# Kernel optimization log

Hardware: AMD Instinct MI355X
Metric: run time of the kernel (lower is better)

The kernel has to match this reference:

```python
import jax, jax.numpy as jnp
import numpy as np

EPS = 1e-5
NUM_CLUSTERS = 64


def _bn(x, g, b, m, v):
    # eval-mode BatchNorm over channel (last) axis
    return (x - m) * (g * jax.lax.rsqrt(v + EPS)) + b


def _segment_max(feat, choice, num_clusters):
    # feat: [B, N, C], choice: [B, N] -> [B, K, C] (amax per cluster, -inf if empty)
    def one(f, c):
        init = jnp.full((num_clusters, f.shape[-1]), -jnp.inf, dtype=f.dtype)
        return init.at[c].max(f)
    return jax.vmap(one)(feat, choice)


def setup_inputs() -> dict:
    key = jax.random.key(0)
    ks = jax.random.split(key, 8)
    B, N, K, OUT = 32, 8192, NUM_CLUSTERS, 384
    s = lambda fan: 1.0 / np.sqrt(fan)
    return {
        "xyz": jax.random.normal(ks[0], (B, N, 3), jnp.float32),
        "choice": jax.random.randint(ks[1], (B, N), 0, K, jnp.int32),
        "w1": jax.random.normal(ks[2], (128, 3), jnp.float32) * s(3),
        "b1": jnp.zeros((128,), jnp.float32),
        "bn1_g": jnp.ones((128,), jnp.float32),
        "bn1_b": jnp.zeros((128,), jnp.float32),
        "bn1_m": jnp.zeros((128,), jnp.float32),
        "bn1_v": jnp.ones((128,), jnp.float32),
        "w2": jax.random.normal(ks[3], (256, 128), jnp.float32) * s(128),
        "b2": jnp.zeros((256,), jnp.float32),
        "w3": jax.random.normal(ks[4], (512, 512), jnp.float32) * s(512),
        "b3": jnp.zeros((512,), jnp.float32),
        "bn2_g": jnp.ones((512,), jnp.float32),
        "bn2_b": jnp.zeros((512,), jnp.float32),
        "bn2_m": jnp.zeros((512,), jnp.float32),
        "bn2_v": jnp.ones((512,), jnp.float32),
        "w4": jax.random.normal(ks[5], (OUT, 512), jnp.float32) * s(512),
        "b4": jnp.zeros((OUT,), jnp.float32),
    }


def reference(xyz, choice, w1, b1, bn1_g, bn1_b, bn1_m, bn1_v, w2, b2,
              w3, b3, bn2_g, bn2_b, bn2_m, bn2_v, w4, b4):
    # first_conv: 1x1 conv == per-point linear. xyz: [B,N,3]
    h = jnp.einsum("bnc,oc->bno", xyz, w1) + b1            # [B,N,128]
    h = jax.nn.relu(_bn(h, bn1_g, bn1_b, bn1_m, bn1_v))
    feat = jnp.einsum("bnc,oc->bno", h, w2) + b2            # [B,N,256]
    # cluster amax pooling + gather-broadcast back to points
    fg = _segment_max(feat, choice, NUM_CLUSTERS)           # [B,K,256]
    fg_pts = jnp.take_along_axis(fg, choice[..., None], axis=1)  # [B,N,256]
    f = jnp.concatenate([fg_pts, feat], axis=-1)            # [B,N,512]
    # second_conv
    h2 = jnp.einsum("bnc,oc->bno", f, w3) + b3              # [B,N,512]
    h2 = jax.nn.relu(_bn(h2, bn2_g, bn2_b, bn2_m, bn2_v))
    out = jnp.einsum("bnc,oc->bno", h2, w4) + b4            # [B,N,out_dim]
    return _segment_max(out, choice, NUM_CLUSTERS)          # [B,K,out_dim]
```

## Files before the change

### kernel.cpp

```cpp
#include <hip/hip_runtime.h>
#include <hip/hip_bf16.h>

typedef unsigned short u16;
typedef __attribute__((ext_vector_type(8))) short short8;
typedef __attribute__((ext_vector_type(4))) float f32x4;

#define EPSV 1e-5f
#define ENC_NINF 0x007FFFFFu

__device__ __forceinline__ float bf2f(u16 u) {
    union { unsigned int i; float f; } v; v.i = ((unsigned int)u) << 16; return v.f;
}
__device__ __forceinline__ u16 f2bf(float f) {
    union { float f; unsigned int i; } v; v.f = f;
    unsigned int x = v.i;
    return (u16)((x + 0x7FFFu + ((x >> 16) & 1u)) >> 16);
}
__device__ __forceinline__ unsigned int encbf(u16 u) {
    unsigned int f = ((unsigned int)u) << 16;
    return (f & 0x80000000u) ? ~f : (f | 0x80000000u);
}
__device__ __forceinline__ float dec(unsigned int u) {
    union { float f; unsigned int uu; } v;
    v.uu = (u & 0x80000000u) ? (u & 0x7FFFFFFFu) : ~u;
    return v.f;
}

__device__ __forceinline__ void async16(const u16* g, u16* l) {
    __builtin_amdgcn_global_load_lds((const __attribute__((address_space(1))) void*)g,
                                     (__attribute__((address_space(3))) void*)l,
                                     16, 0, 0);
}

__global__ __launch_bounds__(256) void k_fillf(float* __restrict__ o, int n, float val)
{
    int i = blockIdx.x * 256 + threadIdx.x;
    if (i < n) o[i] = val;
}

__global__ __launch_bounds__(256) void k_initu(unsigned int* __restrict__ o, int n)
{
    int i = blockIdx.x * 256 + threadIdx.x;
    if (i < n) o[i] = ENC_NINF;
}

struct Ptrs { const void* p[17]; int off[18]; int chN; };

__global__ __launch_bounds__(256) void k_repack(Ptrs P, const void* __restrict__ chSrc,
                                                int* __restrict__ chi, u16* __restrict__ rp)
{
    const unsigned int* probe = (const unsigned int*)P.p[9];
    int cnt = 0;
#pragma unroll
    for (int i = 0; i < 64; ++i) {
        unsigned int lo = probe[i] & 0xFFFFu;
        if (((lo >> 7) & 0xFFu) >= 0x80u) ++cnt;
    }
    const bool is_f32 = (cnt > 8);

    const unsigned int* cp = (const unsigned int*)chSrc;
    int z = 0; unsigned int mx = 0;
    for (int i = 0; i < 1024; ++i) {
        unsigned int w = cp[i];
        z += (w == 0u);
        mx = (w > mx) ? w : mx;
    }
    const int chMode = (mx >= 64u) ? 2 : ((z > 300) ? 1 : 0);

    const int stride = gridDim.x * 256;
    const int gid0 = blockIdx.x * 256 + threadIdx.x;

    const int totalF = P.off[17];
    for (int g = gid0; g < totalF; g += stride) {
        int t = 0;
        while (g >= P.off[t + 1]) ++t;
        int off = g - P.off[t];
        u16 v;
        if (is_f32) v = f2bf(((const float*)P.p[t])[off]);
        else        v = ((const u16*)P.p[t])[off];
        rp[g] = v;
    }
    for (int i = gid0; i < P.chN; i += stride) {
        int v;
        if (chMode == 1)      v = (int)((const long long*)chSrc)[i];
        else if (chMode == 2) v = (int)((const float*)chSrc)[i];
        else                  v = ((const int*)chSrc)[i];
        chi[i] = v & 63;
    }
}

__global__ __launch_bounds__(256) void k_sort(const int* __restrict__ chi,
                                              int* __restrict__ schoice,
                                              int* __restrict__ perm)
{
    __shared__ int hist[64];
    __shared__ int base[64];
    const int b = blockIdx.x, tid = threadIdx.x;
    if (tid < 64) hist[tid] = 0;
    __syncthreads();
    const int o = b << 13;
    for (int i = tid; i < 8192; i += 256) atomicAdd(&hist[chi[o + i]], 1);
    __syncthreads();
    if (tid == 0) {
        int s = 0;
        for (int k = 0; k < 64; ++k) { base[k] = s; s += hist[k]; }
    }
    __syncthreads();
    for (int i = tid; i < 8192; i += 256) {
        int k = chi[o + i];
        int pos = atomicAdd(&base[k], 1);
        schoice[o + pos] = k;
        perm[o + pos] = o + i;
    }
}

__global__ __launch_bounds__(256, 2) void g1_feat(
    const u16* __restrict__ xyz, const u16* __restrict__ w1, const u16* __restrict__ b1,
    const u16* __restrict__ g1v, const u16* __restrict__ bb1,
    const u16* __restrict__ m1, const u16* __restrict__ v1,
    const u16* __restrict__ w2, const u16* __restrict__ b2,
    const int* __restrict__ schoice, const int* __restrict__ perm,
    u16* __restrict__ feat, unsigned int* __restrict__ fg_u)
{
    __shared__ __align__(16) u16 Bs[128 * 128];
    __shared__ unsigned int lred[64 * 128];
    __shared__ float4 pw[128];
    __shared__ float xs[128], ys[128], zs[128];
    __shared__ int chs[128];
    const int tid = threadIdx.x, lane = tid & 63, wave = tid >> 6;
    const int wm = (wave & 1) << 6, wn = (wave >> 1) << 6;
    const int m0 = blockIdx.x << 7, n0 = blockIdx.y << 7;
    if (tid < 128) {
        float s = bf2f(g1v[tid]) * rsqrtf(bf2f(v1[tid]) + EPSV);
        float4 w;
        w.x = bf2f(w1[tid * 3 + 0]) * s;
        w.y = bf2f(w1[tid * 3 + 1]) * s;
        w.z = bf2f(w1[tid * 3 + 2]) * s;
        w.w = (bf2f(b1[tid]) - bf2f(m1[tid])) * s + bf2f(bb1[tid]);
        pw[tid] = w;
        const u16* p = xyz + (size_t)perm[m0 + tid] * 3;
        xs[tid] = bf2f(p[0]); ys[tid] = bf2f(p[1]); zs[tid] = bf2f(p[2]);
        chs[tid] = schoice[m0 + tid];
    }
    const int q = lane >> 4, mr = lane & 15;
    f32x4 acc[4][4] = {};
#pragma unroll
    for (int i = 0; i < 8; ++i) {
        int id = (i << 8) + tid, row = id >> 4, cc = id & 15;
        async16(w2 + (n0 + row) * 128 + ((cc ^ (row & 15)) << 3), &Bs[id << 3]);
    }
    __syncthreads();
    const int kmin = chs[0], nk = chs[127] - kmin + 1;
    for (int i = tid; i < (nk << 7); i += 256) lred[i] = ENC_NINF;
#pragma unroll
    for (int kk = 0; kk < 4; ++kk) {
        const int lc = kk * 4 + q;
        float4 wv[8];
#pragma unroll
        for (int j = 0; j < 8; ++j) wv[j] = pw[kk * 32 + q * 8 + j];
        short8 af[4], bfr[4];
#pragma unroll
        for (int mi = 0; mi < 4; ++mi) {
            int row = wm + mi * 16 + mr;
            float x = xs[row], y = ys[row], z = zs[row];
#pragma unroll
            for (int j = 0; j < 8; ++j) {
                float val = fmaf(x, wv[j].x, fmaf(y, wv[j].y, fmaf(z, wv[j].z, wv[j].w)));
                af[mi][j] = (short)f2bf(fmaxf(val, 0.0f));
            }
        }
#pragma unroll
        for (int ni = 0; ni < 4; ++ni) {
            int r = wn + ni * 16 + mr;
            bfr[ni] = *(const short8*)&Bs[r * 128 + ((lc ^ (r & 15)) << 3)];
        }
#pragma unroll
        for (int mi = 0; mi < 4; ++mi)
#pragma unroll
            for (int ni = 0; ni < 4; ++ni)
                acc[mi][ni] = __builtin_amdgcn_mfma_f32_16x16x32_bf16(af[mi], bfr[ni], acc[mi][ni], 0, 0, 0);
    }
    __syncthreads();
    const int colb = lane & 15;
#pragma unroll
    for (int ni = 0; ni < 4; ++ni) {
        int nc = wn + (ni << 4) + colb;
        int n = n0 + nc;
        float bv = bf2f(b2[n]);
#pragma unroll
        for (int mi = 0; mi < 4; ++mi) {
            int curk = -1; unsigned int run = 0;
#pragma unroll
            for (int r = 0; r < 4; ++r) {
                int rr = wm + (mi << 4) + (q << 2) + r;
                u16 vb = f2bf(acc[mi][ni][r] + bv);
                feat[(size_t)(m0 + rr) * 256 + n] = vb;
                unsigned int e = encbf(vb);
                int k = chs[rr];
                if (k != curk) {
                    if (curk >= 0) atomicMax(&lred[((curk - kmin) << 7) + nc], run);
                    curk = k; run = e;
                } else run = run > e ? run : e;
            }
            atomicMax(&lred[((curk - kmin) << 7) + nc], run);
        }
    }
    __syncthreads();
    const int bl = m0 >> 13;
    unsigned int* db = fg_u + (size_t)(bl << 6) * 256;
    for (int i = tid; i < (nk << 7); i += 256) {
        unsigned int v = lred[i];
        if (v != ENC_NINF) atomicMax(&db[(kmin + (i >> 7)) * 256 + n0 + (i & 127)], v);
    }
}

__global__ __launch_bounds__(256) void g4_out(
    const u16* __restrict__ A, const u16* __restrict__ Bt,
    const u16* __restrict__ bias, const int* __restrict__ schoice,
    unsigned int* __restrict__ out_u, const int K, const int N)
{
    __shared__ __align__(16) u16 smem[2 * 128 * 64];
    __shared__ int chs[128];
    u16* As = smem;
    u16* Bs = smem + 128 * 64;
    const int tid = threadIdx.x, lane = tid & 63, wave = tid >> 6;
    const int wm = (wave & 1) << 6, wn = (wave >> 1) << 6;
    const int m0 = blockIdx.x << 7, n0 = blockIdx.y << 7;
    const int c = tid & 7, rb = tid >> 3;
    if (tid < 128) chs[tid] = schoice[m0 + tid];
    f32x4 acc[4][4] = {};
    for (int k0 = 0; k0 < K; k0 += 64) {
        __syncthreads();
#pragma unroll
        for (int i = 0; i < 4; ++i) {
            int id = (i << 8) + tid, row = id >> 3, cc = id & 7;
            async16(Bt + (n0 + row) * K + k0 + ((cc ^ (row & 7)) << 3), &Bs[id << 3]);
        }
#pragma unroll
        for (int i = 0; i < 4; ++i) {
            int r = rb + (i << 5);
            async16(A + (size_t)(m0 + r) * K + k0 + ((c ^ (r & 7)) << 3),
                    &As[(((i << 8) + tid) << 3)]);
        }
        __syncthreads();
        const int q = lane >> 4, mr = lane & 15;
#pragma unroll
        for (int kk = 0; kk < 2; ++kk) {
            short8 af[4], bfr[4];
            const int lc = kk * 4 + q;
#pragma unroll
            for (int mi = 0; mi < 4; ++mi) {
                int r = wm + mi * 16 + mr;
                af[mi] = *(const short8*)&As[r * 64 + ((lc ^ (r & 7)) << 3)];
            }
#pragma unroll
            for (int ni = 0; ni < 4; ++ni) {
                int r = wn + ni * 16 + mr;
                bfr[ni] = *(const short8*)&Bs[r * 64 + ((lc ^ (r & 7)) << 3)];
            }
#pragma unroll
            for (int mi = 0; mi < 4; ++mi)
#pragma unroll
                for (int ni = 0; ni < 4; ++ni)
                    acc[mi][ni] = __builtin_amdgcn_mfma_f32_16x16x32_bf16(af[mi], bfr[ni], acc[mi][ni], 0, 0, 0);
        }
    }
    __syncthreads();
    unsigned int* lred = (unsigned int*)smem;
    const int kmin = chs[0], nk = chs[127] - kmin + 1;
    for (int i = tid; i < (nk << 7); i += 256) lred[i] = ENC_NINF;
    __syncthreads();
    const int q = lane >> 4, colb = lane & 15;
#pragma unroll
    for (int ni = 0; ni < 4; ++ni) {
        int nc = wn + (ni << 4) + colb;
        float bv = bf2f(bias[n0 + nc]);
#pragma unroll
        for (int mi = 0; mi < 4; ++mi) {
            int curk = -1; unsigned int run = 0;
#pragma unroll
            for (int r = 0; r < 4; ++r) {
                int rr = wm + (mi << 4) + (q << 2) + r;
                unsigned int e = encbf(f2bf(acc[mi][ni][r] + bv));
                int k = chs[rr];
                if (k != curk) {
                    if (curk >= 0) atomicMax(&lred[((curk - kmin) << 7) + nc], run);
                    curk = k; run = e;
                } else run = run > e ? run : e;
            }
            atomicMax(&lred[((curk - kmin) << 7) + nc], run);
        }
    }
    __syncthreads();
    const int bl = m0 >> 13;
    unsigned int* db = out_u + (size_t)(bl << 6) * N;
    for (int i = tid; i < (nk << 7); i += 256) {
        unsigned int v = lred[i];
        if (v != ENC_NINF) atomicMax(&db[(kmin + (i >> 7)) * N + n0 + (i & 127)], v);
    }
}

__global__ __launch_bounds__(256) void k_dec_bf(const unsigned int* __restrict__ u,
                                                u16* __restrict__ o, int n)
{
    int i = blockIdx.x * 256 + threadIdx.x;
    if (i < n) o[i] = f2bf(dec(u[i]));
}
__global__ __launch_bounds__(256) void k_dec_f32(const unsigned int* __restrict__ u,
                                                 float* __restrict__ o, int n)
{
    int i = blockIdx.x * 256 + threadIdx.x;
    if (i < n) o[i] = dec(u[i]);
}

__global__ __launch_bounds__(256, 2) void g3_h2(
    const int* __restrict__ schoice, const u16* __restrict__ feat,
    const u16* __restrict__ fg, const u16* __restrict__ w3, const u16* __restrict__ b3,
    const u16* __restrict__ g2, const u16* __restrict__ bb2,
    const u16* __restrict__ m2, const u16* __restrict__ v2,
    u16* __restrict__ h2)
{
    __shared__ __align__(16) u16 As[128 * 64];
    __shared__ __align__(16) u16 Bs[2 * 128 * 64];
    const int tid = threadIdx.x, lane = tid & 63, wave = tid >> 6;
    const int wm = (wave & 1) << 6, wn = (wave >> 1) << 6;
    const int m0 = blockIdx.x << 7, n0 = blockIdx.y << 8;
    const int c = tid & 7, rb = tid >> 3;
    const u16* fgrow[4]; const u16* ftrow[4];
#pragma unroll
    for (int i = 0; i < 4; ++i) {
        int pt = m0 + rb + (i << 5);
        int b = pt >> 13;
        fgrow[i] = fg + (((b << 6) + schoice[pt]) << 8);
        ftrow[i] = feat + ((size_t)pt << 8);
    }
    f32x4 acc[2][4][4] = {};
    for (int k0 = 0; k0 < 512; k0 += 64) {
        __syncthreads();
#pragma unroll
        for (int nt = 0; nt < 2; ++nt)
#pragma unroll
            for (int i = 0; i < 4; ++i) {
                int id = (i << 8) + tid, row = id >> 3, cc = id & 7;
                async16(w3 + (n0 + nt * 128 + row) * 512 + k0 + ((cc ^ (row & 7)) << 3),
                        &Bs[nt * 8192 + (id << 3)]);
            }
#pragma unroll
        for (int i = 0; i < 4; ++i) {
            int r = rb + (i << 5);
            int col = k0 + ((c ^ (r & 7)) << 3);
            const u16* src = (col < 256) ? (fgrow[i] + col) : (ftrow[i] + (col - 256));
            async16(src, &As[(((i << 8) + tid) << 3)]);
        }
        __syncthreads();
        const int q = lane >> 4, mr = lane & 15;
#pragma unroll
        for (int kk = 0; kk < 2; ++kk) {
            short8 af[4];
            const int lc = kk * 4 + q;
#pragma unroll
            for (int mi = 0; mi < 4; ++mi) {
                int r = wm + mi * 16 + mr;
                af[mi] = *(const short8*)&As[r * 64 + ((lc ^ (r & 7)) << 3)];
            }
#pragma unroll
            for (int nt = 0; nt < 2; ++nt) {
                short8 bfr[4];
#pragma unroll
                for (int ni = 0; ni < 4; ++ni) {
                    int r = wn + ni * 16 + mr;
                    bfr[ni] = *(const short8*)&Bs[nt * 8192 + r * 64 + ((lc ^ (r & 7)) << 3)];
                }
#pragma unroll
                for (int mi = 0; mi < 4; ++mi)
#pragma unroll
                    for (int ni = 0; ni < 4; ++ni)
                        acc[nt][mi][ni] = __builtin_amdgcn_mfma_f32_16x16x32_bf16(af[mi], bfr[ni], acc[nt][mi][ni], 0, 0, 0);
            }
        }
    }
    const int q = lane >> 4, colb = lane & 15;
#pragma unroll
    for (int nt = 0; nt < 2; ++nt)
#pragma unroll
        for (int ni = 0; ni < 4; ++ni) {
            int n = n0 + nt * 128 + wn + (ni << 4) + colb;
            float s = bf2f(g2[n]) * rsqrtf(bf2f(v2[n]) + EPSV);
            float t = (bf2f(b3[n]) - bf2f(m2[n])) * s + bf2f(bb2[n]);
#pragma unroll
            for (int mi = 0; mi < 4; ++mi)
#pragma unroll
                for (int r = 0; r < 4; ++r) {
                    int m = m0 + wm + (mi << 4) + (q << 2) + r;
                    h2[(size_t)m * 512 + n] = f2bf(fmaxf(fmaf(acc[nt][mi][ni][r], s, t), 0.0f));
                }
        }
}

extern "C" void kernel_launch(void* const* d_in, const int* in_sizes, int n_in,
                              void* d_out, int out_size, void* d_ws, size_t ws_size,
                              hipStream_t stream)
{
    float* out = (float*)d_out;
    if (n_in != 18) {
        k_fillf<<<dim3((out_size + 255) / 256), 256, 0, stream>>>(out, out_size, 1000.0f);
        return;
    }

    const int map[17] = {0, 2, 3, 4, 5, 6, 7, 8, 9, 10, 11, 12, 13, 14, 15, 16, 17};
    Ptrs P;
    P.off[0] = 0;
    for (int i = 0; i < 17; ++i) {
        P.p[i] = d_in[map[i]];
        P.off[i + 1] = P.off[i] + in_sizes[map[i]];
    }
    P.chN = in_sizes[1];

    char* ws = (char*)d_ws;
    int* chi = (int*)ws;
    const size_t chiB = ((size_t)P.chN * 4 + 255) & ~255ull;
    int* schoice = (int*)(ws + chiB);
    int* perm    = (int*)(ws + 2 * chiB);
    u16* rp = (u16*)(ws + 3 * chiB);
    const size_t rpB = ((size_t)P.off[17] * 2 + 255) & ~255ull;
    const size_t RPB = 3 * chiB + rpB;

    k_repack<<<dim3(1024), 256, 0, stream>>>(P, d_in[1], chi, rp);
    k_sort<<<dim3(P.chN >> 13), 256, 0, stream>>>(chi, schoice, perm);

    const u16* xyz  = rp + P.off[0];
    const u16* w1   = rp + P.off[1];
    const u16* b1   = rp + P.off[2];
    const u16* bn1g = rp + P.off[3];
    const u16* bn1b = rp + P.off[4];
    const u16* bn1m = rp + P.off[5];
    const u16* bn1v = rp + P.off[6];
    const u16* w2   = rp + P.off[7];
    const u16* b2   = rp + P.off[8];
    const u16* w3   = rp + P.off[9];
    const u16* b3   = rp + P.off[10];
    const u16* bn2g = rp + P.off[11];
    const u16* bn2b = rp + P.off[12];
    const u16* bn2m = rp + P.off[13];
    const u16* bn2v = rp + P.off[14];
    const u16* w4   = rp + P.off[15];
    const u16* b4   = rp + P.off[16];

    const size_t PB = 12779520ull;
    int sb = 32;
    while (sb > 1 && RPB + (size_t)sb * PB > ws_size) sb >>= 1;
    if (RPB + PB > ws_size) {
        k_fillf<<<dim3((out_size + 255) / 256), 256, 0, stream>>>(out, out_size, 3000.0f);
        return;
    }
    const int ns = 32 / sb;

    char* wsb = ws + RPB;
    const size_t featB = (size_t)sb * 8192 * 256 * 2;
    const size_t h2B   = (size_t)sb * 8192 * 512 * 2;
    const size_t fgB   = (size_t)sb * 64 * 256 * 2;
    const size_t fguB  = (size_t)sb * 64 * 256 * 4;
    u16* feat = (u16*)(wsb);
    u16* h2s  = (u16*)(wsb + featB);
    u16* fg   = (u16*)(wsb + featB + h2B);
    unsigned int* fg_u  = (unsigned int*)(wsb + featB + h2B + fgB);
    unsigned int* out_u = (unsigned int*)(wsb + featB + h2B + fgB + fguB);

    const int mblk = sb << 6;
    const int nfg = sb * 64 * 256;
    const int nou = sb * 64 * 384;
    for (int s = 0; s < ns; ++s) {
        const int b0 = s * sb;
        const int pt0 = b0 << 13;
        const int* sch_sl = schoice + pt0;
        const int* perm_sl = perm + pt0;
        k_initu<<<dim3((nfg + nou + 255) / 256), 256, 0, stream>>>(fg_u, nfg + nou);
        g1_feat<<<dim3(mblk, 2), 256, 0, stream>>>(xyz, w1, b1, bn1g, bn1b, bn1m, bn1v,
                                                   w2, b2, sch_sl, perm_sl, feat, fg_u);
        k_dec_bf<<<dim3((nfg + 255) / 256), 256, 0, stream>>>(fg_u, fg, nfg);
        g3_h2<<<dim3(mblk, 2), 256, 0, stream>>>(sch_sl, feat, fg, w3, b3,
                                                 bn2g, bn2b, bn2m, bn2v, h2s);
        g4_out<<<dim3(mblk, 3), 256, 0, stream>>>(h2s, w4, b4, sch_sl, out_u, 512, 384);
        k_dec_f32<<<dim3((nou + 255) / 256), 256, 0, stream>>>(out_u,
                                                               out + ((size_t)b0 << 6) * 384, nou);
    }
}
```

Measured before the change: 526.7 us.

## Precompute per-cluster fg·W3 product and halve the h2 GEMM reduction depth

Because every point in a cluster shares the same pooled feature, the fg half of the concatenated input times W3 is computed once per cluster in a new small kernel (fgw, fp32, with bias folded in). The main h2 GEMM then reduces only over the 256 per-point feature channels and adds the cached per-cluster row in the epilogue, read from LDS when the tile spans few clusters and from global memory otherwise. This removes half of the MFMA work and the gathered A loads, at the cost of an extra launch, extra workspace and per-element epilogue lookups.

```diff
diff --git a/kernel.cpp b/kernel.cpp
--- a/kernel.cpp
+++ b/kernel.cpp
@@ -214,6 +214,31 @@
     }
 }
 
+__global__ __launch_bounds__(256) void k_fgw(const u16* __restrict__ fg,
+                                             const u16* __restrict__ w3,
+                                             const u16* __restrict__ b3,
+                                             float* __restrict__ fgw)
+{
+    __shared__ float fgr[256];
+    const int bk = blockIdx.x, tid = threadIdx.x;
+    fgr[tid] = bf2f(fg[(size_t)bk * 256 + tid]);
+    __syncthreads();
+#pragma unroll
+    for (int half = 0; half < 2; ++half) {
+        int n = half * 256 + tid;
+        const u16* wr = w3 + (size_t)n * 512;
+        float s = 0.0f;
+#pragma unroll
+        for (int c8 = 0; c8 < 256; c8 += 8) {
+            short8 wv = *(const short8*)&wr[c8];
+#pragma unroll
+            for (int j = 0; j < 8; ++j)
+                s = fmaf(fgr[c8 + j], bf2f((u16)wv[j]), s);
+        }
+        fgw[(size_t)bk * 512 + n] = s + bf2f(b3[n]);
+    }
+}
+
 __global__ __launch_bounds__(256) void g4_out(
     const u16* __restrict__ A, const u16* __restrict__ Bt,
     const u16* __restrict__ bias, const int* __restrict__ schoice,
@@ -315,42 +340,46 @@
 
 __global__ __launch_bounds__(256, 2) void g3_h2(
     const int* __restrict__ schoice, const u16* __restrict__ feat,
-    const u16* __restrict__ fg, const u16* __restrict__ w3, const u16* __restrict__ b3,
+    const float* __restrict__ fgw, const u16* __restrict__ w3,
     const u16* __restrict__ g2, const u16* __restrict__ bb2,
     const u16* __restrict__ m2, const u16* __restrict__ v2,
     u16* __restrict__ h2)
 {
     __shared__ __align__(16) u16 As[128 * 64];
     __shared__ __align__(16) u16 Bs[2 * 128 * 64];
+    __shared__ float fgwl[8 * 256];
+    __shared__ int chs[128];
     const int tid = threadIdx.x, lane = tid & 63, wave = tid >> 6;
     const int wm = (wave & 1) << 6, wn = (wave >> 1) << 6;
-    const int m0 = blockIdx.x << 7, n0 = blockIdx.y << 8;
+    const int m0 = blockIdx.x << 7, n0g = blockIdx.y << 8;
     const int c = tid & 7, rb = tid >> 3;
-    const u16* fgrow[4]; const u16* ftrow[4];
-#pragma unroll
-    for (int i = 0; i < 4; ++i) {
-        int pt = m0 + rb + (i << 5);
-        int b = pt >> 13;
-        fgrow[i] = fg + (((b << 6) + schoice[pt]) << 8);
-        ftrow[i] = feat + ((size_t)pt << 8);
+    const int bl = m0 >> 13;
+    if (tid < 128) chs[tid] = schoice[m0 + tid];
+    __syncthreads();
+    const int kmin = chs[0], nk = chs[127] - kmin + 1;
+    const bool cached = (nk <= 8);
+    if (cached) {
+        for (int i = tid; i < (nk << 8); i += 256) {
+            int k = kmin + (i >> 8);
+            fgwl[i] = fgw[(size_t)((bl << 6) + k) * 512 + n0g + (i & 255)];
+        }
     }
     f32x4 acc[2][4][4] = {};
-    for (int k0 = 0; k0 < 512; k0 += 64) {
+    for (int k0 = 0; k0 < 256; k0 += 64) {
         __syncthreads();
 #pragma unroll
         for (int nt = 0; nt < 2; ++nt)
 #pragma unroll
             for (int i = 0; i < 4; ++i) {
                 int id = (i << 8) + tid, row = id >> 3, cc = id & 7;
-                async16(w3 + (n0 + nt * 128 + row) * 512 + k0 + ((cc ^ (row & 7)) << 3),
+                async16(w3 + (size_t)(n0g + nt * 128 + row) * 512 + 256 + k0 + ((cc ^ (row & 7)) << 3),
                         &Bs[nt * 8192 + (id << 3)]);
             }
 #pragma unroll
         for (int i = 0; i < 4; ++i) {
             int r = rb + (i << 5);
-            int col = k0 + ((c ^ (r & 7)) << 3);
-            const u16* src = (col < 256) ? (fgrow[i] + col) : (ftrow[i] + (col - 256));
-            async16(src, &As[(((i << 8) + tid) << 3)]);
+            async16(feat + (size_t)(m0 + r) * 256 + k0 + ((c ^ (r & 7)) << 3),
+                    &As[(((i << 8) + tid) << 3)]);
         }
         __syncthreads();
         const int q = lane >> 4, mr = lane & 15;
@@ -384,15 +413,20 @@
     for (int nt = 0; nt < 2; ++nt)
 #pragma unroll
         for (int ni = 0; ni < 4; ++ni) {
-            int n = n0 + nt * 128 + wn + (ni << 4) + colb;
+            int nc = nt * 128 + wn + (ni << 4) + colb;
+            int n = n0g + nc;
             float s = bf2f(g2[n]) * rsqrtf(bf2f(v2[n]) + EPSV);
-            float t = (bf2f(b3[n]) - bf2f(m2[n])) * s + bf2f(bb2[n]);
+            float t2 = bf2f(bb2[n]) - bf2f(m2[n]) * s;
 #pragma unroll
             for (int mi = 0; mi < 4; ++mi)
 #pragma unroll
                 for (int r = 0; r < 4; ++r) {
-                    int m = m0 + wm + (mi << 4) + (q << 2) + r;
-                    h2[(size_t)m * 512 + n] = f2bf(fmaxf(fmaf(acc[nt][mi][ni][r], s, t), 0.0f));
+                    int rr = wm + (mi << 4) + (q << 2) + r;
+                    int k = chs[rr];
+                    float fgv = cached ? fgwl[((k - kmin) << 8) + nc]
+                                       : fgw[(size_t)((bl << 6) + k) * 512 + n];
+                    float raw = acc[nt][mi][ni][r] + fgv;
+                    h2[(size_t)(m0 + rr) * 512 + n] = f2bf(fmaxf(fmaf(raw, s, t2), 0.0f));
                 }
         }
 }
@@ -446,7 +480,7 @@
     const u16* w4   = rp + P.off[15];
     const u16* b4   = rp + P.off[16];
 
-    const size_t PB = 12779520ull;
+    const size_t PB = 12910592ull;
     int sb = 32;
     while (sb > 1 && RPB + (size_t)sb * PB > ws_size) sb >>= 1;
     if (RPB + PB > ws_size) {
@@ -460,11 +494,14 @@
     const size_t h2B   = (size_t)sb * 8192 * 512 * 2;
     const size_t fgB   = (size_t)sb * 64 * 256 * 2;
     const size_t fguB  = (size_t)sb * 64 * 256 * 4;
+    const size_t fgwB  = (size_t)sb * 64 * 512 * 4;
     u16* feat = (u16*)(wsb);
     u16* h2s  = (u16*)(wsb + featB);
     u16* fg   = (u16*)(wsb + featB + h2B);
     unsigned int* fg_u  = (unsigned int*)(wsb + featB + h2B + fgB);
     unsigned int* out_u = (unsigned int*)(wsb + featB + h2B + fgB + fguB);
+    float* fgw = (float*)(wsb + featB + h2B + fgB + fguB + (size_t)sb * 64 * 384 * 4);
+    (void)fgwB;
 
     const int mblk = sb << 6;
     const int nfg = sb * 64 * 256;
@@ -478,7 +515,8 @@
         g1_feat<<<dim3(mblk, 2), 256, 0, stream>>>(xyz, w1, b1, bn1g, bn1b, bn1m, bn1v,
                                                    w2, b2, sch_sl, perm_sl, feat, fg_u);
         k_dec_bf<<<dim3((nfg + 255) / 256), 256, 0, stream>>>(fg_u, fg, nfg);
-        g3_h2<<<dim3(mblk, 2), 256, 0, stream>>>(sch_sl, feat, fg, w3, b3,
+        k_fgw<<<dim3(sb * 64), 256, 0, stream>>>(fg, w3, b3, fgw);
+        g3_h2<<<dim3(mblk, 2), 256, 0, stream>>>(sch_sl, feat, fgw, w3,
                                                  bn2g, bn2b, bn2m, bn2v, h2s);
         g4_out<<<dim3(mblk, 3), 256, 0, stream>>>(h2s, w4, b4, sch_sl, out_u, 512, 384);
         k_dec_f32<<<dim3((nou + 255) / 256), 256, 0, stream>>>(out_u,
```

Result: slower. 711.9 us (+35.1%).

## Compute all 256 feat columns per g1 block and hoist atomic buffer init

Applied to the files above, without the earlier changes.

g1_feat now computes all 256 output channels per block, loading all of w2 into LDS, so the first-layer xyz transform is computed once per point instead of twice. The LDS reduction buffer is reshaped to 8 clusters × 256 channels, falling back to global atomics when a block spans more clusters. The per-slice init kernel is replaced by one init over a shared atomic buffer for all batches, and launch bounds for g3 and g4 are raised to request more occupancy. The cost is more LDS and accumulator registers per g1 block, and possible register spills in g3 and g4 under the tighter bounds.

```diff
diff --git a/kernel.cpp b/kernel.cpp
--- a/kernel.cpp
+++ b/kernel.cpp
@@ -122,14 +122,14 @@
     const int* __restrict__ schoice, const int* __restrict__ perm,
     u16* __restrict__ feat, unsigned int* __restrict__ fg_u)
 {
-    __shared__ __align__(16) u16 Bs[128 * 128];
-    __shared__ unsigned int lred[64 * 128];
+    __shared__ __align__(16) u16 Bs[256 * 128];
+    __shared__ unsigned int lred[8 * 256];
     __shared__ float4 pw[128];
     __shared__ float xs[128], ys[128], zs[128];
     __shared__ int chs[128];
     const int tid = threadIdx.x, lane = tid & 63, wave = tid >> 6;
     const int wm = (wave & 1) << 6, wn = (wave >> 1) << 6;
-    const int m0 = blockIdx.x << 7, n0 = blockIdx.y << 7;
+    const int m0 = blockIdx.x << 7;
     if (tid < 128) {
         float s = bf2f(g1v[tid]) * rsqrtf(bf2f(v1[tid]) + EPSV);
         float4 w;
@@ -143,22 +143,23 @@
         chs[tid] = schoice[m0 + tid];
     }
     const int q = lane >> 4, mr = lane & 15;
-    f32x4 acc[4][4] = {};
-#pragma unroll
-    for (int i = 0; i < 8; ++i) {
+    f32x4 acc[2][4][4] = {};
+#pragma unroll
+    for (int i = 0; i < 16; ++i) {
         int id = (i << 8) + tid, row = id >> 4, cc = id & 15;
-        async16(w2 + (n0 + row) * 128 + ((cc ^ (row & 15)) << 3), &Bs[id << 3]);
+        async16(w2 + (size_t)row * 128 + ((cc ^ (row & 15)) << 3), &Bs[id << 3]);
     }
     __syncthreads();
     const int kmin = chs[0], nk = chs[127] - kmin + 1;
-    for (int i = tid; i < (nk << 7); i += 256) lred[i] = ENC_NINF;
+    const bool useL = (nk <= 8);
+    if (useL) for (int i = tid; i < (nk << 8); i += 256) lred[i] = ENC_NINF;
 #pragma unroll
     for (int kk = 0; kk < 4; ++kk) {
         const int lc = kk * 4 + q;
         float4 wv[8];
 #pragma unroll
         for (int j = 0; j < 8; ++j) wv[j] = pw[kk * 32 + q * 8 + j];
-        short8 af[4], bfr[4];
+        short8 af[4];
 #pragma unroll
         for (int mi = 0; mi < 4; ++mi) {
             int row = wm + mi * 16 + mr;
@@ -170,51 +171,62 @@
             }
         }
 #pragma unroll
-        for (int ni = 0; ni < 4; ++ni) {
-            int r = wn + ni * 16 + mr;
-            bfr[ni] = *(const short8*)&Bs[r * 128 + ((lc ^ (r & 15)) << 3)];
-        }
-#pragma unroll
-        for (int mi = 0; mi < 4; ++mi)
-#pragma unroll
-            for (int ni = 0; ni < 4; ++ni)
-                acc[mi][ni] = __builtin_amdgcn_mfma_f32_16x16x32_bf16(af[mi], bfr[ni], acc[mi][ni], 0, 0, 0);
+        for (int h = 0; h < 2; ++h) {
+            short8 bfr[4];
+#pragma unroll
+            for (int ni = 0; ni < 4; ++ni) {
+                int r = (h << 7) + wn + ni * 16 + mr;
+                bfr[ni] = *(const short8*)&Bs[r * 128 + ((lc ^ (r & 15)) << 3)];
+            }
+#pragma unroll
+            for (int mi = 0; mi < 4; ++mi)
+#pragma unroll
+                for (int ni = 0; ni < 4; ++ni)
+                    acc[h][mi][ni] = __builtin_amdgcn_mfma_f32_16x16x32_bf16(af[mi], bfr[ni], acc[h][mi][ni], 0, 0, 0);
+        }
     }
     __syncthreads();
     const int colb = lane & 15;
-#pragma unroll
-    for (int ni = 0; ni < 4; ++ni) {
-        int nc = wn + (ni << 4) + colb;
-        int n = n0 + nc;
-        float bv = bf2f(b2[n]);
-#pragma unroll
-        for (int mi = 0; mi < 4; ++mi) {
-            int curk = -1; unsigned int run = 0;
-#pragma unroll
-            for (int r = 0; r < 4; ++r) {
-                int rr = wm + (mi << 4) + (q << 2) + r;
-                u16 vb = f2bf(acc[mi][ni][r] + bv);
-                feat[(size_t)(m0 + rr) * 256 + n] = vb;
-                unsigned int e = encbf(vb);
-                int k = chs[rr];
-                if (k != curk) {
-                    if (curk >= 0) atomicMax(&lred[((curk - kmin) << 7) + nc], run);
-                    curk = k; run = e;
-                } else run = run > e ? run : e;
-            }
-            atomicMax(&lred[((curk - kmin) << 7) + nc], run);
-        }
-    }
-    __syncthreads();
     const int bl = m0 >> 13;
     unsigned int* db = fg_u + (size_t)(bl << 6) * 256;
-    for (int i = tid; i < (nk << 7); i += 256) {
-        unsigned int v = lred[i];
-        if (v != ENC_NINF) atomicMax(&db[(kmin + (i >> 7)) * 256 + n0 + (i & 127)], v);
-    }
-}
-
-__global__ __launch_bounds__(256) void g4_out(
+#pragma unroll
+    for (int h = 0; h < 2; ++h)
+#pragma unroll
+        for (int ni = 0; ni < 4; ++ni) {
+            int n = (h << 7) + wn + (ni << 4) + colb;
+            float bv = bf2f(b2[n]);
+#pragma unroll
+            for (int mi = 0; mi < 4; ++mi) {
+                int curk = -1; unsigned int run = 0;
+#pragma unroll
+                for (int r = 0; r < 4; ++r) {
+                    int rr = wm + (mi << 4) + (q << 2) + r;
+                    u16 vb = f2bf(acc[h][mi][ni][r] + bv);
+                    feat[(size_t)(m0 + rr) * 256 + n] = vb;
+                    unsigned int e = encbf(vb);
+                    int k = chs[rr];
+                    if (k != curk) {
+                        if (curk >= 0) {
+                            if (useL) atomicMax(&lred[((curk - kmin) << 8) + n], run);
+                            else      atomicMax(&db[curk * 256 + n], run);
+                        }
+                        curk = k; run = e;
+                    } else run = run > e ? run : e;
+                }
+                if (useL) atomicMax(&lred[((curk - kmin) << 8) + n], run);
+                else      atomicMax(&db[curk * 256 + n], run);
+            }
+        }
+    if (useL) {
+        __syncthreads();
+        for (int i = tid; i < (nk << 8); i += 256) {
+            unsigned int v = lred[i];
+            if (v != ENC_NINF) atomicMax(&db[(kmin + (i >> 8)) * 256 + (i & 255)], v);
+        }
+    }
+}
+
+__global__ __launch_bounds__(256, 4) void g4_out(
     const u16* __restrict__ A, const u16* __restrict__ Bt,
     const u16* __restrict__ bias, const int* __restrict__ schoice,
     unsigned int* __restrict__ out_u, const int K, const int N)
@@ -313,7 +325,7 @@
     if (i < n) o[i] = dec(u[i]);
 }
 
-__global__ __launch_bounds__(256, 2) void g3_h2(
+__global__ __launch_bounds__(256, 3) void g3_h2(
     const int* __restrict__ schoice, const u16* __restrict__ feat,
     const u16* __restrict__ fg, const u16* __restrict__ w3, const u16* __restrict__ b3,
     const u16* __restrict__ g2, const u16* __restrict__ bb2,
@@ -342,7 +354,7 @@
 #pragma unroll
             for (int i = 0; i < 4; ++i) {
                 int id = (i << 8) + tid, row = id >> 3, cc = id & 7;
-                async16(w3 + (n0 + nt * 128 + row) * 512 + k0 + ((cc ^ (row & 7)) << 3),
+                async16(w3 + (size_t)(n0 + nt * 128 + row) * 512 + k0 + ((cc ^ (row & 7)) << 3),
                         &Bs[nt * 8192 + (id << 3)]);
             }
 #pragma unroll
@@ -446,25 +458,28 @@
     const u16* w4   = rp + P.off[15];
     const u16* b4   = rp + P.off[16];
 
-    const size_t PB = 12779520ull;
+    unsigned int* fg_u_all  = (unsigned int*)(ws + RPB);
+    unsigned int* out_u_all = fg_u_all + 32 * 64 * 256;
+    const size_t UB = 5242880ull;
+    const int nU = 32 * 64 * 640;
+
+    const size_t PB = 12615680ull;
     int sb = 32;
-    while (sb > 1 && RPB + (size_t)sb * PB > ws_size) sb >>= 1;
-    if (RPB + PB > ws_size) {
+    while (sb > 1 && RPB + UB + (size_t)sb * PB > ws_size) sb >>= 1;
+    if (RPB + UB + PB > ws_size) {
         k_fillf<<<dim3((out_size + 255) / 256), 256, 0, stream>>>(out, out_size, 3000.0f);
         return;
     }
     const int ns = 32 / sb;
 
-    char* wsb = ws + RPB;
+    char* wsb = ws + RPB + UB;
     const size_t featB = (size_t)sb * 8192 * 256 * 2;
     const size_t h2B   = (size_t)sb * 8192 * 512 * 2;
-    const size_t fgB   = (size_t)sb * 64 * 256 * 2;
-    const size_t fguB  = (size_t)sb * 64 * 256 * 4;
     u16* feat = (u16*)(wsb);
     u16* h2s  = (u16*)(wsb + featB);
     u16* fg   = (u16*)(wsb + featB + h2B);
-    unsigned int* fg_u  = (unsigned int*)(wsb + featB + h2B + fgB);
-    unsigned int* out_u = (unsigned int*)(wsb + featB + h2B + fgB + fguB);
+
+    k_initu<<<dim3((nU + 255) / 256), 256, 0, stream>>>(fg_u_all, nU);
 
     const int mblk = sb << 6;
     const int nfg = sb * 64 * 256;
@@ -474,9 +489,10 @@
         const int pt0 = b0 << 13;
         const int* sch_sl = schoice + pt0;
         const int* perm_sl = perm + pt0;
-        k_initu<<<dim3((nfg + nou + 255) / 256), 256, 0, stream>>>(fg_u, nfg + nou);
-        g1_feat<<<dim3(mblk, 2), 256, 0, stream>>>(xyz, w1, b1, bn1g, bn1b, bn1m, bn1v,
-                                                   w2, b2, sch_sl, perm_sl, feat, fg_u);
+        unsigned int* fg_u  = fg_u_all + (size_t)b0 * 64 * 256;
+        unsigned int* out_u = out_u_all + (size_t)b0 * 64 * 384;
+        g1_feat<<<dim3(mblk), 256, 0, stream>>>(xyz, w1, b1, bn1g, bn1b, bn1m, bn1v,
+                                                w2, b2, sch_sl, perm_sl, feat, fg_u);
         k_dec_bf<<<dim3((nfg + 255) / 256), 256, 0, stream>>>(fg_u, fg, nfg);
         g3_h2<<<dim3(mblk, 2), 256, 0, stream>>>(sch_sl, feat, fg, w3, b3,
                                                  bn2g, bn2b, bn2m, bn2v, h2s);
```

After: 769.1 us. 1.46x slower.
